# Performance work log

Measured on AMD Instinct MI355X. Metric: run time of the kernel, lower is better.

The kernel has to match this reference:

```python
import jax, jax.numpy as jnp
import numpy as np

EMB_DIM = 1024
NUM_HEADS = 16
HEAD_DIM = EMB_DIM // NUM_HEADS  # 64
B, S = 2, 2048


def setup_inputs() -> dict:
    key = jax.random.key(0)
    ks = jax.random.split(key, 9)
    scale = 1.0 / np.sqrt(EMB_DIM)
    return {
        "query": jax.random.normal(ks[0], (B, S, EMB_DIM), dtype=jnp.float32),
        "Wq": jax.random.normal(ks[1], (EMB_DIM, EMB_DIM), dtype=jnp.float32) * scale,
        "bq": jax.random.normal(ks[2], (EMB_DIM,), dtype=jnp.float32) * 0.01,
        "Wk": jax.random.normal(ks[3], (EMB_DIM, EMB_DIM), dtype=jnp.float32) * scale,
        "bk": jax.random.normal(ks[4], (EMB_DIM,), dtype=jnp.float32) * 0.01,
        "Wv": jax.random.normal(ks[5], (EMB_DIM, EMB_DIM), dtype=jnp.float32) * scale,
        "bv": jax.random.normal(ks[6], (EMB_DIM,), dtype=jnp.float32) * 0.01,
        "Wo": jax.random.normal(ks[7], (EMB_DIM, EMB_DIM), dtype=jnp.float32) * scale,
        "bo": jax.random.normal(ks[8], (EMB_DIM,), dtype=jnp.float32) * 0.01,
    }


def reference(query, Wq, bq, Wk, bk, Wv, bv, Wo, bo):
    # Self-attention path (key_value=None, mask=None in the original forward).
    b, s, _ = query.shape
    # torch nn.Linear: y = x @ W.T + b
    def proj(x, W, bias):
        y = jnp.einsum('bse,fe->bsf', x, W) + bias
        # [B,S,E] -> [B,H,S,D]
        return y.reshape(b, s, NUM_HEADS, HEAD_DIM).transpose(0, 2, 1, 3)

    q = proj(query, Wq, bq)
    k = proj(query, Wk, bk)
    v = proj(query, Wv, bv)

    scores = jnp.einsum('bhqd,bhkd->bhqk', q, k) / np.sqrt(HEAD_DIM).astype(np.float32)
    attn = jax.nn.softmax(scores, axis=-1)  # [B,H,S,S]
    out = jnp.einsum('bhqk,bhkd->bhqd', attn, v)
    out = out.transpose(0, 2, 1, 3).reshape(b, s, EMB_DIM)
    return jnp.einsum('bse,fe->bsf', out, Wo) + bo
```

## Files before the change

kernel.cpp:

```cpp
#include <hip/hip_runtime.h>
#include <hip/hip_bf16.h>

using bf16x4 = __attribute__((ext_vector_type(4))) short;
using short8 = __attribute__((ext_vector_type(8))) short;
using f32x4  = __attribute__((ext_vector_type(4))) float;
using f32x16 = __attribute__((ext_vector_type(16))) float;
using u32x2  = __attribute__((ext_vector_type(2))) unsigned;

__device__ __forceinline__ short f2bf(float f) {
  unsigned u = __builtin_bit_cast(unsigned, f);
  u = (u + 0x7fffu + ((u >> 16) & 1u)) >> 16;
  return (short)u;
}
__device__ __forceinline__ unsigned pk2(float a, float b) {
  __hip_bfloat162 h = __float22bfloat162_rn(make_float2(a, b));
  unsigned u; __builtin_memcpy(&u, &h, 4);
  return u;
}
__device__ __forceinline__ void gload16(const short* g, short* l) {
  __builtin_amdgcn_global_load_lds(
      (const __attribute__((address_space(1))) unsigned int*)g,
      (__attribute__((address_space(3))) unsigned int*)l, 16, 0, 0);
}
__device__ __forceinline__ void pl32swap(unsigned &a, unsigned &b) {
  asm("v_permlane32_swap_b32 %0, %1" : "+v"(a), "+v"(b));
}

constexpr int E  = 1024;
constexpr int SL = 2048;
constexpr int NB = 2;
constexpr int NH = 16;
constexpr int M  = NB * SL;

__global__ __launch_bounds__(256) void convert_kernel(
    const float* __restrict__ X,  const float* __restrict__ Wq,
    const float* __restrict__ Wk, const float* __restrict__ Wv,
    const float* __restrict__ Wo, short* __restrict__ out)
{
  const size_t i8 = ((size_t)blockIdx.x * 256 + threadIdx.x) * 8;
  const float* src;
  if (i8 < (size_t)(4u << 20)) {
    src = X + i8;
  } else {
    size_t r = i8 - (size_t)(4u << 20);
    int wi = (int)(r >> 20);
    size_t off = r & ((1u << 20) - 1);
    src = (wi == 0 ? Wq : wi == 1 ? Wk : wi == 2 ? Wv : Wo) + off;
  }
  f32x4 a = *(const f32x4*)src;
  f32x4 b = *(const f32x4*)(src + 4);
  short hb[8];
#pragma unroll
  for (int e = 0; e < 4; ++e) { hb[e] = f2bf(a[e]); hb[4 + e] = f2bf(b[e]); }
  *(short8*)(out + i8) = *(short8*)hb;
}

template <bool OUTF32, bool PROJ>
__device__ __forceinline__ void gemm_body(
    const short* __restrict__ A0, const short* __restrict__ A1, const short* __restrict__ A2,
    const short* __restrict__ B0, const short* __restrict__ B1, const short* __restrict__ B2,
    const float* __restrict__ b0, const float* __restrict__ b1, const float* __restrict__ b2,
    void* __restrict__ Y0, void* __restrict__ Y1, void* __restrict__ Y2,
    float s0, float s1, float s2, int ld0, int ld1, int ld2)
{
  constexpr int BK = 32;
  constexpr int TM = 128, TN = 128;
  constexpr int RA = TM / 64;
  constexpr int RB = TN / 64;
  constexpr int WM = TM / 2, WN = TN / 2;
  constexpr int NI = WM / 16, NJ = WN / 16;
  __shared__ alignas(16) short As[2][TM * BK];
  __shared__ alignas(16) short Bs[2][TN * BK];
  const int t = threadIdx.x;
  const int l = t & 63;
  const int w = t >> 6;
  const int c = l & 15;
  const int g = l >> 4;

  const int fid = (int)blockIdx.x;
  int z, m0, n0;
  if (PROJ) {
    const int orig = (fid & 7) * 96 + (fid >> 3);
    z = orig >> 8;
    const int rem = orig & 255;
    const bool sw = (z != 2);
    m0 = (sw ? (rem >> 5) : (rem & 31)) * TM;
    n0 = (sw ? (rem & 31) : (rem >> 5)) * TN;
  } else {
    const int orig = (fid & 7) * 32 + (fid >> 3);
    z = 0;
    m0 = (orig >> 5) * TM;
    n0 = (orig & 31) * TN;
  }
  const short* Ap = (z == 0) ? A0 : (z == 1) ? A1 : A2;
  const short* Bp = (z == 0) ? B0 : (z == 1) ? B1 : B2;
  const float* bp = (z == 0) ? b0 : (z == 1) ? b1 : b2;
  void* Yp        = (z == 0) ? Y0 : (z == 1) ? Y1 : Y2;
  const float sc  = (z == 0) ? s0 : (z == 1) ? s1 : s2;
  const int ldY   = (z == 0) ? ld0 : (z == 1) ? ld1 : ld2;
  const bool swp  = PROJ ? (z != 2) : true;

  const short* gA[RA]; int oA[RA];
  const short* gB[RB]; int oB[RB];
#pragma unroll
  for (int r = 0; r < RA; ++r) {
    const int cc = r * 256 + t;
    gA[r] = Ap + (size_t)(m0 + (cc >> 2)) * E + (cc & 3) * 8;
    oA[r] = (r * 256 + (t & ~63)) * 8;
  }
#pragma unroll
  for (int r = 0; r < RB; ++r) {
    const int cc = r * 256 + t;
    gB[r] = Bp + (size_t)(n0 + (cc >> 2)) * E + (cc & 3) * 8;
    oB[r] = (r * 256 + (t & ~63)) * 8;
  }

#pragma unroll
  for (int r = 0; r < RA; ++r) gload16(gA[r], &As[0][oA[r]]);
#pragma unroll
  for (int r = 0; r < RB; ++r) gload16(gB[r], &Bs[0][oB[r]]);

  const int wm = (w >> 1) * WM;
  const int wn = (w & 1) * WN;
  f32x4 acc[NI][NJ] = {};
  int cur = 0;

  for (int k0 = 0; k0 < E; k0 += BK) {
    __syncthreads();
    if (k0 + BK < E) {
#pragma unroll
      for (int r = 0; r < RA; ++r) gload16(gA[r] + k0 + BK, &As[cur ^ 1][oA[r]]);
#pragma unroll
      for (int r = 0; r < RB; ++r) gload16(gB[r] + k0 + BK, &Bs[cur ^ 1][oB[r]]);
    }
    short8 ah[NI], bfr[NJ];
#pragma unroll
    for (int i = 0; i < NI; ++i)
      ah[i] = *(const short8*)&As[cur][(wm + i * 16 + c) * BK + g * 8];
#pragma unroll
    for (int j = 0; j < NJ; ++j)
      bfr[j] = *(const short8*)&Bs[cur][(wn + j * 16 + c) * BK + g * 8];
#pragma unroll
    for (int i = 0; i < NI; ++i)
#pragma unroll
      for (int j = 0; j < NJ; ++j)
        acc[i][j] = __builtin_amdgcn_mfma_f32_16x16x32_bf16(ah[i], bfr[j], acc[i][j], 0, 0, 0);
    cur ^= 1;
  }

  float bm[NI][4];
  if (swp) {
#pragma unroll
    for (int i = 0; i < NI; ++i)
#pragma unroll
      for (int r = 0; r < 4; ++r)
        bm[i][r] = bp[m0 + wm + i * 16 + g * 4 + r];
  }
#pragma unroll
  for (int j = 0; j < NJ; ++j) {
    const int col = n0 + wn + j * 16 + c;
    const float bj = swp ? 0.f : bp[col];
#pragma unroll
    for (int i = 0; i < NI; ++i) {
      const int row = m0 + wm + i * 16 + g * 4;
      float v[4];
#pragma unroll
      for (int r = 0; r < 4; ++r)
        v[r] = (acc[i][j][r] + (swp ? bm[i][r] : bj)) * sc;
      if (OUTF32) {
        f32x4 o = {v[0], v[1], v[2], v[3]};
        *(f32x4*)((float*)Yp + (size_t)col * ldY + row) = o;
      } else {
        u32x2 o = {pk2(v[0], v[1]), pk2(v[2], v[3])};
        *(u32x2*)((short*)Yp + (size_t)col * ldY + row) = o;
      }
    }
  }
}

__global__ __launch_bounds__(256) void proj_kernel(
    const short* A0, const short* A1, const short* A2,
    const short* B0, const short* B1, const short* B2,
    const float* b0, const float* b1, const float* b2,
    void* Y0, void* Y1, void* Y2,
    float s0, float s1, float s2, int ld0, int ld1, int ld2)
{
  gemm_body<false, true>(A0, A1, A2, B0, B1, B2, b0, b1, b2,
                         Y0, Y1, Y2, s0, s1, s2, ld0, ld1, ld2);
}

__global__ __launch_bounds__(256) void out_kernel(
    const short* A0, const short* A1, const short* A2,
    const short* B0, const short* B1, const short* B2,
    const float* b0, const float* b1, const float* b2,
    void* Y0, void* Y1, void* Y2,
    float s0, float s1, float s2, int ld0, int ld1, int ld2)
{
  gemm_body<true, false>(A0, A1, A2, B0, B1, B2, b0, b1, b2,
                         Y0, Y1, Y2, s0, s1, s2, ld0, ld1, ld2);
}

__global__ __launch_bounds__(256, 2) void flash_kernel(
    const short* __restrict__ Qm, const short* __restrict__ Km,
    const short* __restrict__ VTm, short* __restrict__ Oh)
{
  __shared__ alignas(16) short Ks[2][64][64];
  __shared__ alignas(16) short Vt[2][64][64];
  const int t = threadIdx.x;
  const int l = t & 63;
  const int w = t >> 6;
  const int c = l & 31;
  const int hi = l >> 5;
  const int fid = (int)blockIdx.x;
  const int orig = (fid & 7) * 64 + (fid >> 3);
  const int q0 = (orig & 15) * 128;
  const int bh = orig >> 4;
  const int bat = bh >> 4;
  const int h = bh & 15;
  const size_t baseK = (size_t)bat * SL * E + h * 64;
  const size_t baseV = (size_t)(h * 64) * M + (size_t)bat * SL;

  short8 qf[4];
  {
    const short* qp = Qm + baseK + (size_t)(q0 + w * 32 + c) * E + hi * 8;
#pragma unroll
    for (int tt = 0; tt < 4; ++tt) qf[tt] = *(const short8*)(qp + tt * 16);
  }

  const int sr = t >> 3, sg = t & 7;
  const int swz = (sg ^ (sr & 7)) * 8;
  const short* gK0 = Km + baseK + (size_t)sr * E + sg * 8;
  const short* gK1 = gK0 + (size_t)32 * E;
  const short* gV0 = VTm + baseV + (size_t)sr * M + sg * 8;
  const short* gV1 = gV0 + (size_t)32 * M;
  const int wo0 = sr * 64 + swz;
  const int wo1 = (sr + 32) * 64 + swz;

  short8 k0r, k1r, v0r, v1r;
  k0r = *(const short8*)gK0; k1r = *(const short8*)gK1;
  v0r = *(const short8*)gV0; v1r = *(const short8*)gV1;
  *(short8*)(&Ks[0][0][0] + wo0) = k0r; *(short8*)(&Ks[0][0][0] + wo1) = k1r;
  *(short8*)(&Vt[0][0][0] + wo0) = v0r; *(short8*)(&Vt[0][0][0] + wo1) = v1r;
  k0r = *(const short8*)(gK0 + (size_t)64 * E);
  k1r = *(const short8*)(gK1 + (size_t)64 * E);
  v0r = *(const short8*)(gV0 + 64);
  v1r = *(const short8*)(gV1 + 64);

  f32x16 oa0 = {}, oa1 = {};
  f32x4 lacc = {0.f, 0.f, 0.f, 0.f};
  __syncthreads();

  constexpr int NTT = SL / 64;
  const int sx = c & 7;
  for (int kt = 0; kt < NTT; ++kt) {
    const int cur = kt & 1;
    if (kt + 1 < NTT) {
      short* Kn = &Ks[cur ^ 1][0][0];
      short* Vn = &Vt[cur ^ 1][0][0];
      *(short8*)(Kn + wo0) = k0r; *(short8*)(Kn + wo1) = k1r;
      *(short8*)(Vn + wo0) = v0r; *(short8*)(Vn + wo1) = v1r;
      if (kt + 2 < NTT) {
        const size_t ko = (size_t)(kt + 2) * 64 * E;
        const int vo = (kt + 2) * 64;
        k0r = *(const short8*)(gK0 + ko); k1r = *(const short8*)(gK1 + ko);
        v0r = *(const short8*)(gV0 + vo); v1r = *(const short8*)(gV1 + vo);
      }
    }
    const short* Kc0 = &Ks[cur][c][0];
    const short* Kc1 = &Ks[cur][32 + c][0];
    const short* Vc0 = &Vt[cur][c][0];
    const short* Vc1 = &Vt[cur][32 + c][0];

    f32x16 st0 = {}, st1 = {};
    __builtin_amdgcn_s_setprio(1);
#pragma unroll
    for (int tt = 0; tt < 4; ++tt) {
      const int off = ((tt * 2 + hi) ^ sx) * 8;
      short8 kf0 = *(const short8*)(Kc0 + off);
      short8 kf1 = *(const short8*)(Kc1 + off);
      st0 = __builtin_amdgcn_mfma_f32_32x32x16_bf16(kf0, qf[tt], st0, 0, 0, 0);
      st1 = __builtin_amdgcn_mfma_f32_32x32x16_bf16(kf1, qf[tt], st1, 0, 0, 0);
    }
    __builtin_amdgcn_s_setprio(0);

    float p0[16], p1[16];
#pragma unroll
    for (int i = 0; i < 16; ++i) p0[i] = __builtin_amdgcn_exp2f(st0[i]);
#pragma unroll
    for (int i = 0; i < 16; ++i) p1[i] = __builtin_amdgcn_exp2f(st1[i]);
#pragma unroll
    for (int i = 0; i < 16; ++i) lacc[i & 3] += p0[i] + p1[i];

    unsigned W0[4][2], W1[4][2];
#pragma unroll
    for (int b8 = 0; b8 < 4; ++b8) {
      W0[b8][0] = pk2(p0[4 * b8 + 0], p0[4 * b8 + 1]);
      W0[b8][1] = pk2(p0[4 * b8 + 2], p0[4 * b8 + 3]);
      W1[b8][0] = pk2(p1[4 * b8 + 0], p1[4 * b8 + 1]);
      W1[b8][1] = pk2(p1[4 * b8 + 2], p1[4 * b8 + 3]);
    }

    __builtin_amdgcn_s_setprio(1);
#pragma unroll
    for (int tt = 0; tt < 4; ++tt) {
      unsigned a0, a1, b0, b1;
      if (tt == 0)      { a0 = W0[0][0]; a1 = W0[0][1]; b0 = W0[1][0]; b1 = W0[1][1]; }
      else if (tt == 1) { a0 = W0[2][0]; a1 = W0[2][1]; b0 = W0[3][0]; b1 = W0[3][1]; }
      else if (tt == 2) { a0 = W1[0][0]; a1 = W1[0][1]; b0 = W1[1][0]; b1 = W1[1][1]; }
      else              { a0 = W1[2][0]; a1 = W1[2][1]; b0 = W1[3][0]; b1 = W1[3][1]; }
      pl32swap(a0, b0);
      pl32swap(a1, b1);
      union { unsigned u[4]; short8 s8; } pf;
      pf.u[0] = a0; pf.u[1] = a1; pf.u[2] = b0; pf.u[3] = b1;
      const int off = ((tt * 2 + hi) ^ sx) * 8;
      short8 vf0 = *(const short8*)(Vc0 + off);
      short8 vf1 = *(const short8*)(Vc1 + off);
      oa0 = __builtin_amdgcn_mfma_f32_32x32x16_bf16(vf0, pf.s8, oa0, 0, 0, 0);
      oa1 = __builtin_amdgcn_mfma_f32_32x32x16_bf16(vf1, pf.s8, oa1, 0, 0, 0);
    }
    __builtin_amdgcn_s_setprio(0);
    __syncthreads();
  }

  float s = lacc[0] + lacc[1] + lacc[2] + lacc[3];
  s += __shfl_xor(s, 32);
  const float inv = 1.0f / s;
  const int q = q0 + w * 32 + c;
  short* op = Oh + ((size_t)bat * SL + q) * E + h * 64 + hi * 4;
#pragma unroll
  for (int b8 = 0; b8 < 4; ++b8) {
    u32x2 t0 = {pk2(oa0[4 * b8 + 0] * inv, oa0[4 * b8 + 1] * inv),
                pk2(oa0[4 * b8 + 2] * inv, oa0[4 * b8 + 3] * inv)};
    *(u32x2*)(op + b8 * 8) = t0;
    u32x2 t1 = {pk2(oa1[4 * b8 + 0] * inv, oa1[4 * b8 + 1] * inv),
                pk2(oa1[4 * b8 + 2] * inv, oa1[4 * b8 + 3] * inv)};
    *(u32x2*)(op + 32 + b8 * 8) = t1;
  }
}

extern "C" void kernel_launch(void* const* d_in, const int* in_sizes, int n_in,
                              void* d_out, int out_size, void* d_ws, size_t ws_size,
                              hipStream_t stream)
{
  const float* X  = (const float*)d_in[0];
  const float* Wq = (const float*)d_in[1];
  const float* bq = (const float*)d_in[2];
  const float* Wk = (const float*)d_in[3];
  const float* bk = (const float*)d_in[4];
  const float* Wv = (const float*)d_in[5];
  const float* bv = (const float*)d_in[6];
  const float* Wo = (const float*)d_in[7];
  const float* bo = (const float*)d_in[8];
  float* out = (float*)d_out;

  const size_t szX = (size_t)M * E;
  const size_t szW = (size_t)E * E;
  short* Xb  = (short*)d_ws;
  short* Wqb = Xb + szX;
  short* Wkb = Wqb + szW;
  short* Wvb = Wkb + szW;
  short* Wob = Wvb + szW;
  short* Qw  = Wob + szW;
  short* Kw  = Qw + szX;
  short* VTw = Kw + szX;

  convert_kernel<<<4096, 256, 0, stream>>>(X, Wq, Wk, Wv, Wo, Xb);

  const float kLog2eOver8 = 0.18033688011112042f;
  proj_kernel<<<768, 256, 0, stream>>>(
      Wqb, Wkb, Xb,
      Xb, Xb, Wvb,
      bq, bk, bv,
      (void*)Qw, (void*)Kw, (void*)VTw,
      kLog2eOver8, 1.0f, 1.0f, E, E, M);

  flash_kernel<<<512, 256, 0, stream>>>(Qw, Kw, VTw, Qw );

  out_kernel<<<256, 256, 0, stream>>>(
      Wob, Wob, Wob,
      Qw, Qw, Qw,
      bo, bo, bo,
      (void*)out, (void*)out, (void*)out,
      1.0f, 1.0f, 1.0f, E, E, E);
}
```

Baseline: 192.3 us.

## Halve flash-attention block to 2 waves over 64 queries, doubling grid

The flash attention kernel now runs 128 threads (2 waves) per block, each block covering 64 query rows instead of 128, and the grid doubles to 1024 blocks. Each thread loads and stores 4 K/V rows per tile instead of 2 to keep the 64-row tile fill intact, and the block-to-(batch,head,q-tile) remapping is adjusted. The aim is better load balance and occupancy across CUs with a larger grid. The cost is twice the K/V global-to-LDS traffic per query, since each K/V tile is now reused by fewer query rows, plus more per-thread load registers.

```diff
diff --git a/kernel.cpp b/kernel.cpp
--- a/kernel.cpp
+++ b/kernel.cpp
@@ -200,7 +200,7 @@
                          Y0, Y1, Y2, s0, s1, s2, ld0, ld1, ld2);
 }
 
-__global__ __launch_bounds__(256, 2) void flash_kernel(
+__global__ __launch_bounds__(128, 2) void flash_kernel(
     const short* __restrict__ Qm, const short* __restrict__ Km,
     const short* __restrict__ VTm, short* __restrict__ Oh)
 {
@@ -212,9 +212,9 @@
   const int c = l & 31;
   const int hi = l >> 5;
   const int fid = (int)blockIdx.x;
-  const int orig = (fid & 7) * 64 + (fid >> 3);
-  const int q0 = (orig & 15) * 128;
-  const int bh = orig >> 4;
+  const int orig = (fid & 7) * 128 + (fid >> 3);
+  const int q0 = (orig & 31) * 64;
+  const int bh = orig >> 5;
   const int bat = bh >> 4;
   const int h = bh & 15;
   const size_t baseK = (size_t)bat * SL * E + h * 64;
@@ -229,22 +229,28 @@
 
   const int sr = t >> 3, sg = t & 7;
   const int swz = (sg ^ (sr & 7)) * 8;
-  const short* gK0 = Km + baseK + (size_t)sr * E + sg * 8;
-  const short* gK1 = gK0 + (size_t)32 * E;
-  const short* gV0 = VTm + baseV + (size_t)sr * M + sg * 8;
-  const short* gV1 = gV0 + (size_t)32 * M;
-  const int wo0 = sr * 64 + swz;
-  const int wo1 = (sr + 32) * 64 + swz;
-
-  short8 k0r, k1r, v0r, v1r;
-  k0r = *(const short8*)gK0; k1r = *(const short8*)gK1;
-  v0r = *(const short8*)gV0; v1r = *(const short8*)gV1;
-  *(short8*)(&Ks[0][0][0] + wo0) = k0r; *(short8*)(&Ks[0][0][0] + wo1) = k1r;
-  *(short8*)(&Vt[0][0][0] + wo0) = v0r; *(short8*)(&Vt[0][0][0] + wo1) = v1r;
-  k0r = *(const short8*)(gK0 + (size_t)64 * E);
-  k1r = *(const short8*)(gK1 + (size_t)64 * E);
-  v0r = *(const short8*)(gV0 + 64);
-  v1r = *(const short8*)(gV1 + 64);
+  const short* gK[4]; const short* gV[4]; int wo[4];
+#pragma unroll
+  for (int r = 0; r < 4; ++r) {
+    const int row = r * 16 + sr;
+    gK[r] = Km + baseK + (size_t)row * E + sg * 8;
+    gV[r] = VTm + baseV + (size_t)row * M + sg * 8;
+    wo[r] = row * 64 + swz;
+  }
+
+  short8 kr[4], vr[4];
+#pragma unroll
+  for (int r = 0; r < 4; ++r) { kr[r] = *(const short8*)gK[r]; vr[r] = *(const short8*)gV[r]; }
+#pragma unroll
+  for (int r = 0; r < 4; ++r) {
+    *(short8*)(&Ks[0][0][0] + wo[r]) = kr[r];
+    *(short8*)(&Vt[0][0][0] + wo[r]) = vr[r];
+  }
+#pragma unroll
+  for (int r = 0; r < 4; ++r) {
+    kr[r] = *(const short8*)(gK[r] + (size_t)64 * E);
+    vr[r] = *(const short8*)(gV[r] + 64);
+  }
 
   f32x16 oa0 = {}, oa1 = {};
   f32x4 lacc = {0.f, 0.f, 0.f, 0.f};
@@ -257,13 +263,19 @@
     if (kt + 1 < NTT) {
       short* Kn = &Ks[cur ^ 1][0][0];
       short* Vn = &Vt[cur ^ 1][0][0];
-      *(short8*)(Kn + wo0) = k0r; *(short8*)(Kn + wo1) = k1r;
-      *(short8*)(Vn + wo0) = v0r; *(short8*)(Vn + wo1) = v1r;
+#pragma unroll
+      for (int r = 0; r < 4; ++r) {
+        *(short8*)(Kn + wo[r]) = kr[r];
+        *(short8*)(Vn + wo[r]) = vr[r];
+      }
       if (kt + 2 < NTT) {
         const size_t ko = (size_t)(kt + 2) * 64 * E;
         const int vo = (kt + 2) * 64;
-        k0r = *(const short8*)(gK0 + ko); k1r = *(const short8*)(gK1 + ko);
-        v0r = *(const short8*)(gV0 + vo); v1r = *(const short8*)(gV1 + vo);
+#pragma unroll
+        for (int r = 0; r < 4; ++r) {
+          kr[r] = *(const short8*)(gK[r] + ko);
+          vr[r] = *(const short8*)(gV[r] + vo);
+        }
       }
     }
     const short* Kc0 = &Ks[cur][c][0];
@@ -374,7 +386,7 @@
       (void*)Qw, (void*)Kw, (void*)VTw,
       kLog2eOver8, 1.0f, 1.0f, E, E, M);
 
-  flash_kernel<<<512, 256, 0, stream>>>(Qw, Kw, VTw, Qw );
+  flash_kernel<<<1024, 128, 0, stream>>>(Qw, Kw, VTw, Qw );
 
   out_kernel<<<256, 256, 0, stream>>>(
       Wob, Wob, Wob,
```

After: 203.8 us. 1.06x slower.
